# Kernel optimization log

Measured on AMD Instinct MI355X. Metric: run time of the kernel, lower is better.

Reference implementation:

```python
import jax, jax.numpy as jnp
import numpy as np

# Fixed 5-node star graph (edges 0->1,0->2,0->3,0->4) with self-loops,
# GCN symmetric normalization: M[t,s] = deg^-1/2[t] * deg^-1/2[s] over A+I.
# In-degrees: node0 = 1 (self-loop only), nodes 1..4 = 2 (self + edge from 0).
def _prop_matrix():
    M = np.zeros((5, 5), dtype=np.float32)
    M[0, 0] = 1.0
    inv_sqrt2 = 1.0 / np.sqrt(2.0)
    for k in range(1, 5):
        M[k, k] = 0.5            # self-loop: (1/sqrt2)*(1/sqrt2)
        M[k, 0] = inv_sqrt2      # edge 0->k: (1/sqrt1)*(1/sqrt2)
    return jnp.asarray(M)

_M = _prop_matrix()


def _gcn(x, W1, b1, W2, b2):
    # x: [..., 5, 21] node features for batched 5-node graphs
    h = jnp.einsum('ts,...sd->...td', _M, x @ W1) + b1   # [..., 5, 128]
    h = jax.nn.relu(h)
    o = jnp.einsum('ts,...sd->...td', _M, h @ W2) + b2   # [..., 5, 21]
    return o


def setup_inputs() -> dict:
    key = jax.random.key(0)
    k1, k2, k3, k4, k5 = jax.random.split(key, 5)
    B, H, W = 4, 256, 256
    instance_nodes = jax.random.randint(k1, (B, H, W, 5), 0, 129, dtype=jnp.int64)
    class_nodes = jax.random.randint(k2, (21, 5), 0, 129, dtype=jnp.int64)
    emb = jax.random.normal(k3, (129, 21), dtype=jnp.float32)
    emb = emb.at[128].set(0.0)  # padding_idx=128 row is zero
    W1 = jax.random.normal(k4, (21, 128), dtype=jnp.float32) * 0.1
    b1 = jnp.zeros((128,), dtype=jnp.float32)
    W2 = jax.random.normal(k5, (128, 21), dtype=jnp.float32) * 0.1
    b2 = jnp.zeros((21,), dtype=jnp.float32)
    return {"instance_nodes": instance_nodes, "class_nodes": class_nodes,
            "emb": emb, "W1": W1, "b1": b1, "W2": W2, "b2": b2}


def reference(instance_nodes, class_nodes, emb, W1, b1, W2, b2):
    B, H, W, n = instance_nodes.shape
    # class branch: 21 tiny graphs -> [21, 105]
    x_class = emb[class_nodes]                     # [21, 5, 21]
    out_class = _gcn(x_class, W1, b1, W2, b2).reshape(21, 105)
    # instance branch: B*H*W tiny graphs, fully batched
    x_inst = emb[instance_nodes]                   # [B, H, W, 5, 21]
    out_inst = _gcn(x_inst, W1, b1, W2, b2).reshape(B, H, W, 105)
    # inner-product similarity against each class vector
    sim = jnp.einsum('bhwf,cf->bhwc', out_inst, out_class)  # [B, H, W, 21]
    return sim
```

## Files before the change

### kernel.cpp

```cpp
#include <hip/hip_runtime.h>


#define IS2 0.70710678118654752440f

constexpr int NE  = 129;
constexpr int D1  = 128;
constexpr int DF  = 21;
constexpr int NC  = 21;
constexpr int ROWA = 24;

constexpr int U_OFF   = 0;
constexpr int GT_OFF  = U_OFF  + NE * D1;
constexpr int A_OFF   = GT_OFF + D1 * 84;
constexpr int OC_OFF  = A_OFF  + NE * ROWA;
constexpr int S_OFF   = OC_OFF + NC * 105;
constexpr int G0_OFF  = S_OFF  + NC * DF;
constexpr int CST_OFF = G0_OFF + NC * D1;
constexpr int P_OFF   = ((CST_OFF + NC + 31) / 32) * 32;
constexpr long long P_ELEMS32 = 4LL * NE * NE * 32;

constexpr int BT  = 16;
constexpr int NBT = (NE + BT - 1) / BT;

__global__ __launch_bounds__(D1) void k_u(const float* __restrict__ emb,
                                          const float* __restrict__ W1,
                                          float* __restrict__ u) {
    int i = blockIdx.x;
    int j = threadIdx.x;
    __shared__ float e[DF];
    if (threadIdx.x < DF) e[threadIdx.x] = emb[i * DF + threadIdx.x];
    __syncthreads();
    float acc = 0.f;
#pragma unroll
    for (int k = 0; k < DF; ++k) acc += e[k] * W1[k * D1 + j];
    u[i * D1 + j] = acc;
}

__global__ __launch_bounds__(D1) void k_class_a(const int* __restrict__ cn,
                                                const float* __restrict__ b1,
                                                const float* __restrict__ W2,
                                                const float* __restrict__ b2,
                                                float* __restrict__ ws) {
    const float* u = ws + U_OFF;
    float* oc  = ws + OC_OFF;
    float* S   = ws + S_OFF;
    float* cst = ws + CST_OFF;

    const int c   = blockIdx.x;
    const int tid = threadIdx.x;

    __shared__ float h[5 * D1];
    __shared__ float v[5 * DF];
    __shared__ float ocs[105];
    __shared__ float Ss[DF];

    const int n0 = cn[c * 5];
#pragma unroll
    for (int s = 0; s < 5; ++s) {
        int ns = cn[c * 5 + s];
        float pre = (s == 0) ? (u[n0 * D1 + tid] + b1[tid])
                             : (IS2 * u[n0 * D1 + tid] + 0.5f * u[ns * D1 + tid] + b1[tid]);
        h[s * D1 + tid] = fmaxf(pre, 0.f);
    }
    __syncthreads();

    if (tid < 105) {
        int s = tid / DF, j = tid % DF;
        const float* hs = h + s * D1;
        float a0 = 0.f, a1 = 0.f;
#pragma unroll 8
        for (int k = 0; k < D1; k += 2) {
            a0 += hs[k]     * W2[k * DF + j];
            a1 += hs[k + 1] * W2[(k + 1) * DF + j];
        }
        v[tid] = a0 + a1;
    }
    __syncthreads();

    if (tid < 105) {
        int t = tid / DF, j = tid % DF;
        float v0 = v[j];
        float val = (t == 0) ? (v0 + b2[j])
                             : (IS2 * v0 + 0.5f * v[t * DF + j] + b2[j]);
        ocs[tid] = val;
        oc[c * 105 + tid] = val;
    }
    __syncthreads();

    if (tid < DF) {
        float sv = ocs[21 + tid] + ocs[42 + tid] + ocs[63 + tid] + ocs[84 + tid];
        Ss[tid] = sv;
        S[c * DF + tid] = sv;
    }
    __syncthreads();

    if (tid == 0) {
        float acc = 0.f;
#pragma unroll
        for (int j = 0; j < DF; ++j) acc += b2[j] * (ocs[j] + Ss[j]);
        cst[c] = acc;
    }
}

__global__ __launch_bounds__(256) void k_class_b(const float* __restrict__ W2,
                                                 float* __restrict__ ws) {
    const float* oc = ws + OC_OFF;
    const float* S  = ws + S_OFF;
    float* gGt = ws + GT_OFF;
    float* G0  = ws + G0_OFF;

    int idx = blockIdx.x * 256 + threadIdx.x;
    if (idx < D1 * 84) {
        int k = idx / 84, tc = idx % 84;
        int t = tc / DF + 1, c = tc % DF;
        float acc = 0.f;
#pragma unroll
        for (int j = 0; j < DF; ++j) acc += W2[k * DF + j] * oc[c * 105 + t * DF + j];
        gGt[idx] = 0.5f * acc;
    } else if (idx < D1 * 84 + NC * D1) {
        int r = idx - D1 * 84;
        int c = r / D1, k = r % D1;
        float acc = 0.f;
#pragma unroll
        for (int j = 0; j < DF; ++j)
            acc += W2[k * DF + j] * (oc[c * 105 + j] + IS2 * S[c * DF + j]);
        G0[c * D1 + k] = acc;
    }
}

__global__ __launch_bounds__(D1) void k_class_c(const float* __restrict__ b1,
                                                float* __restrict__ ws) {
    const float* u   = ws + U_OFF;
    const float* G0  = ws + G0_OFF;
    const float* cst = ws + CST_OFF;
    float* gA = ws + A_OFF;

    const int n0  = blockIdx.x;
    const int tid = threadIdx.x;

    __shared__ float h0[D1];
    h0[tid] = fmaxf(u[n0 * D1 + tid] + b1[tid], 0.f);
    __syncthreads();

    if (tid < NC) {
        const float* g = G0 + tid * D1;
        float a0 = 0.f, a1 = 0.f;
#pragma unroll 8
        for (int k = 0; k < D1; k += 2) {
            a0 += h0[k]     * g[k];
            a1 += h0[k + 1] * g[k + 1];
        }
        gA[n0 * ROWA + tid] = cst[tid] + a0 + a1;
    }
}

__global__ __launch_bounds__(256) void k_pair(const float* __restrict__ b1,
                                              float* __restrict__ ws, int rowP) {
    const float* u   = ws + U_OFF;
    const float* gGt = ws + GT_OFF;
    float* P         = ws + P_OFF;

    const int a  = blockIdx.x / NBT;
    const int b0 = (blockIdx.x % NBT) * BT;

    __shared__ float ua[D1];
    __shared__ float hp[BT * D1];
    __shared__ float gt[D1 * 84];
    const int tid = threadIdx.x;

    if (tid < D1) ua[tid] = IS2 * u[a * D1 + tid] + b1[tid];
    {
        const float4* src = (const float4*)gGt;
        float4* dst = (float4*)gt;
        for (int i = tid; i < D1 * 84 / 4; i += 256) dst[i] = src[i];
    }
    __syncthreads();

    for (int e = tid; e < BT * D1; e += 256) {
        int p = e / D1, k = e % D1; int b = b0 + p;
        float val = 0.f;
        if (b < NE) val = fmaxf(ua[k] + 0.5f * u[b * D1 + k], 0.f);
        hp[e] = val;
    }
    __syncthreads();

    if (tid < (BT / 2) * 28) {
        const int p0  = (tid / 28) * 2;
        const int tc0 = (tid % 28) * 3;
        const float* hA = hp + p0 * D1;
        const float* hB = hA + D1;

        float e00 = 0.f, e01 = 0.f, e02 = 0.f, e10 = 0.f, e11 = 0.f, e12 = 0.f;
        float o00 = 0.f, o01 = 0.f, o02 = 0.f, o10 = 0.f, o11 = 0.f, o12 = 0.f;
#pragma unroll 4
        for (int k = 0; k < D1; k += 2) {
            float ha0 = hA[k], hb0 = hB[k];
            float ha1 = hA[k + 1], hb1 = hB[k + 1];
            const float* g0 = gt + k * 84 + tc0;
            const float* g1 = g0 + 84;
            float ge0 = g0[0], ge1 = g0[1], ge2 = g0[2];
            float go0 = g1[0], go1 = g1[1], go2 = g1[2];
            e00 += ha0 * ge0; e01 += ha0 * ge1; e02 += ha0 * ge2;
            e10 += hb0 * ge0; e11 += hb0 * ge1; e12 += hb0 * ge2;
            o00 += ha1 * go0; o01 += ha1 * go1; o02 += ha1 * go2;
            o10 += hb1 * go0; o11 += hb1 * go1; o12 += hb1 * go2;
        }

        const int t  = tc0 / DF;
        const int c0 = tc0 - t * DF;
        const long long rbase = (long long)(t * NE * NE + a * NE);
        const int bA = b0 + p0, bB = bA + 1;
        if (bA < NE) {
            float* dst = P + (rbase + bA) * rowP + c0;
            dst[0] = e00 + o00; dst[1] = e01 + o01; dst[2] = e02 + o02;
        }
        if (bB < NE) {
            float* dst = P + (rbase + bB) * rowP + c0;
            dst[0] = e10 + o10; dst[1] = e11 + o11; dst[2] = e12 + o12;
        }
    }
}

__global__ __launch_bounds__(256) void k_main(const int* __restrict__ inst,
                                              const float* __restrict__ ws,
                                              float* __restrict__ out,
                                              long long n_graphs, int rowP) {
    const float* gA = ws + A_OFF;
    const float* P  = ws + P_OFF;

    __shared__ float so[256 * NC];
    __shared__ int   si[256 * 5];
    const int tid = threadIdx.x;
    const long long gbase = (long long)blockIdx.x * 256;
    const bool full = (gbase + 256 <= n_graphs);

    if (full) {
        const int4* src = (const int4*)(inst + gbase * 5);
        int4* dst = (int4*)si;
        for (int i = tid; i < 320; i += 256) dst[i] = src[i];
    } else {
        long long lim = (n_graphs - gbase) * 5;
        for (int i = tid; i < 256 * 5; i += 256)
            si[i] = (i < lim) ? inst[gbase * 5 + i] : 0;
    }
    __syncthreads();

    const long long g = gbase + tid;
    if (g < n_graphs) {
        const int n0 = si[tid * 5 + 0];
        const int n1 = si[tid * 5 + 1];
        const int n2 = si[tid * 5 + 2];
        const int n3 = si[tid * 5 + 3];
        const int n4 = si[tid * 5 + 4];

        const int nn = NE * NE;
        const float4* pa = (const float4*)(gA + n0 * ROWA);
        const float4* p1 = (const float4*)(P + (long long)((0 * nn + n0 * NE + n1)) * rowP);
        const float4* p2 = (const float4*)(P + (long long)((1 * nn + n0 * NE + n2)) * rowP);
        const float4* p3 = (const float4*)(P + (long long)((2 * nn + n0 * NE + n3)) * rowP);
        const float4* p4 = (const float4*)(P + (long long)((3 * nn + n0 * NE + n4)) * rowP);

        float acc[ROWA];
#pragma unroll
        for (int q = 0; q < ROWA / 4; ++q) {
            float4 a0 = pa[q], a1 = p1[q], a2 = p2[q], a3 = p3[q], a4 = p4[q];
            acc[4 * q + 0] = a0.x + a1.x + a2.x + a3.x + a4.x;
            acc[4 * q + 1] = a0.y + a1.y + a2.y + a3.y + a4.y;
            acc[4 * q + 2] = a0.z + a1.z + a2.z + a3.z + a4.z;
            acc[4 * q + 3] = a0.w + a1.w + a2.w + a3.w + a4.w;
        }

#pragma unroll
        for (int c = 0; c < NC; ++c) so[tid * NC + c] = acc[c];
    }
    __syncthreads();

    const long long lim = (n_graphs - gbase) * NC;
    const long long base = gbase * NC;
    for (int i = tid; i < 256 * NC; i += 256)
        if (i < lim) out[base + i] = so[i];
}

extern "C" void kernel_launch(void* const* d_in, const int* in_sizes, int n_in,
                              void* d_out, int out_size, void* d_ws, size_t ws_size,
                              hipStream_t stream) {
    const int*   inst = (const int*)d_in[0];
    const int*   cn   = (const int*)d_in[1];
    const float* emb  = (const float*)d_in[2];
    const float* W1   = (const float*)d_in[3];
    const float* b1   = (const float*)d_in[4];
    const float* W2   = (const float*)d_in[5];
    const float* b2   = (const float*)d_in[6];
    float* out = (float*)d_out;
    float* ws  = (float*)d_ws;

    const long long n_graphs = (long long)in_sizes[0] / 5;
    const int nblk = (int)((n_graphs + 255) / 256);

    const int rowP =
        (ws_size >= (size_t)(P_OFF + P_ELEMS32) * sizeof(float)) ? 32 : 24;

    k_u      <<<dim3(NE),       dim3(D1),  0, stream>>>(emb, W1, ws + U_OFF);
    k_class_a<<<dim3(NC),       dim3(D1),  0, stream>>>(cn, b1, W2, b2, ws);
    k_class_b<<<dim3(53),       dim3(256), 0, stream>>>(W2, ws);
    k_class_c<<<dim3(NE),       dim3(D1),  0, stream>>>(b1, ws);
    k_pair   <<<dim3(NE * NBT), dim3(256), 0, stream>>>(b1, ws, rowP);
    k_main   <<<dim3(nblk),     dim3(256), 0, stream>>>(inst, ws, out, n_graphs, rowP);
}
```

Measured before the change: 144.0 us.

## Split each graph's gather-sum across six threads in main kernel

Changes k_main from one thread per graph (256 graphs per block, staged through shared memory) to six threads per graph (32 graphs per block). Five lanes each gather a float4 from the five precomputed table rows and write their slice of the output directly, and the sixth lane handles the last element. This spreads the random gathers across more threads for more memory-level parallelism and removes the shared-memory output staging. In exchange it issues many more, smaller blocks, makes output stores uncoalesced scalar writes, and leaves some lanes of each wavefront idle.

```diff
diff --git a/kernel.cpp b/kernel.cpp
--- a/kernel.cpp
+++ b/kernel.cpp
@@ -21,6 +21,9 @@
 
 constexpr int BT  = 16;
 constexpr int NBT = (NE + BT - 1) / BT;
+
+constexpr int GPB = 32;
+constexpr int TPG = 6;
 
 __global__ __launch_bounds__(D1) void k_u(const float* __restrict__ emb,
                                           const float* __restrict__ W1,
@@ -221,64 +224,56 @@
     }
 }
 
-__global__ __launch_bounds__(256) void k_main(const int* __restrict__ inst,
-                                              const float* __restrict__ ws,
-                                              float* __restrict__ out,
-                                              long long n_graphs, int rowP) {
+__global__ __launch_bounds__(GPB * TPG) void k_main(const int* __restrict__ inst,
+                                                    const float* __restrict__ ws,
+                                                    float* __restrict__ out,
+                                                    long long n_graphs, int rowP) {
     const float* gA = ws + A_OFF;
     const float* P  = ws + P_OFF;
 
-    __shared__ float so[256 * NC];
-    __shared__ int   si[256 * 5];
+    __shared__ int si[GPB * 5];
     const int tid = threadIdx.x;
-    const long long gbase = (long long)blockIdx.x * 256;
-    const bool full = (gbase + 256 <= n_graphs);
-
-    if (full) {
-        const int4* src = (const int4*)(inst + gbase * 5);
-        int4* dst = (int4*)si;
-        for (int i = tid; i < 320; i += 256) dst[i] = src[i];
+    const long long gbase = (long long)blockIdx.x * GPB;
+
+    if (tid < GPB * 5) {
+        long long lim = (n_graphs - gbase) * 5;
+        si[tid] = (tid < lim) ? inst[gbase * 5 + tid] : 0;
+    }
+    __syncthreads();
+
+    const int gl = tid / TPG;
+    const int q  = tid % TPG;
+    const long long g = gbase + gl;
+    if (g >= n_graphs) return;
+
+    const int n0 = si[gl * 5 + 0];
+    const int n1 = si[gl * 5 + 1];
+    const int n2 = si[gl * 5 + 2];
+    const int n3 = si[gl * 5 + 3];
+    const int n4 = si[gl * 5 + 4];
+
+    const int nn = NE * NE;
+    const float* r0 = gA + n0 * ROWA;
+    const float* r1 = P + (long long)(0 * nn + n0 * NE + n1) * rowP;
+    const float* r2 = P + (long long)(1 * nn + n0 * NE + n2) * rowP;
+    const float* r3 = P + (long long)(2 * nn + n0 * NE + n3) * rowP;
+    const float* r4 = P + (long long)(3 * nn + n0 * NE + n4) * rowP;
+
+    float* og = out + g * NC;
+    if (q < 5) {
+        const int o = q * 4;
+        float4 a0 = *(const float4*)(r0 + o);
+        float4 a1 = *(const float4*)(r1 + o);
+        float4 a2 = *(const float4*)(r2 + o);
+        float4 a3 = *(const float4*)(r3 + o);
+        float4 a4 = *(const float4*)(r4 + o);
+        og[o + 0] = a0.x + a1.x + a2.x + a3.x + a4.x;
+        og[o + 1] = a0.y + a1.y + a2.y + a3.y + a4.y;
+        og[o + 2] = a0.z + a1.z + a2.z + a3.z + a4.z;
+        og[o + 3] = a0.w + a1.w + a2.w + a3.w + a4.w;
     } else {
-        long long lim = (n_graphs - gbase) * 5;
-        for (int i = tid; i < 256 * 5; i += 256)
-            si[i] = (i < lim) ? inst[gbase * 5 + i] : 0;
-    }
-    __syncthreads();
-
-    const long long g = gbase + tid;
-    if (g < n_graphs) {
-        const int n0 = si[tid * 5 + 0];
-        const int n1 = si[tid * 5 + 1];
-        const int n2 = si[tid * 5 + 2];
-        const int n3 = si[tid * 5 + 3];
-        const int n4 = si[tid * 5 + 4];
-
-        const int nn = NE * NE;
-        const float4* pa = (const float4*)(gA + n0 * ROWA);
-        const float4* p1 = (const float4*)(P + (long long)((0 * nn + n0 * NE + n1)) * rowP);
-        const float4* p2 = (const float4*)(P + (long long)((1 * nn + n0 * NE + n2)) * rowP);
-        const float4* p3 = (const float4*)(P + (long long)((2 * nn + n0 * NE + n3)) * rowP);
-        const float4* p4 = (const float4*)(P + (long long)((3 * nn + n0 * NE + n4)) * rowP);
-
-        float acc[ROWA];
-#pragma unroll
-        for (int q = 0; q < ROWA / 4; ++q) {
-            float4 a0 = pa[q], a1 = p1[q], a2 = p2[q], a3 = p3[q], a4 = p4[q];
-            acc[4 * q + 0] = a0.x + a1.x + a2.x + a3.x + a4.x;
-            acc[4 * q + 1] = a0.y + a1.y + a2.y + a3.y + a4.y;
-            acc[4 * q + 2] = a0.z + a1.z + a2.z + a3.z + a4.z;
-            acc[4 * q + 3] = a0.w + a1.w + a2.w + a3.w + a4.w;
-        }
-
-#pragma unroll
-        for (int c = 0; c < NC; ++c) so[tid * NC + c] = acc[c];
-    }
-    __syncthreads();
-
-    const long long lim = (n_graphs - gbase) * NC;
-    const long long base = gbase * NC;
-    for (int i = tid; i < 256 * NC; i += 256)
-        if (i < lim) out[base + i] = so[i];
+        og[20] = r0[20] + r1[20] + r2[20] + r3[20] + r4[20];
+    }
 }
 
 extern "C" void kernel_launch(void* const* d_in, const int* in_sizes, int n_in,
@@ -295,15 +290,15 @@
     float* ws  = (float*)d_ws;
 
     const long long n_graphs = (long long)in_sizes[0] / 5;
-    const int nblk = (int)((n_graphs + 255) / 256);
+    const int nblk_main = (int)((n_graphs + GPB - 1) / GPB);
 
     const int rowP =
         (ws_size >= (size_t)(P_OFF + P_ELEMS32) * sizeof(float)) ? 32 : 24;
 
-    k_u      <<<dim3(NE),       dim3(D1),  0, stream>>>(emb, W1, ws + U_OFF);
-    k_class_a<<<dim3(NC),       dim3(D1),  0, stream>>>(cn, b1, W2, b2, ws);
-    k_class_b<<<dim3(53),       dim3(256), 0, stream>>>(W2, ws);
-    k_class_c<<<dim3(NE),       dim3(D1),  0, stream>>>(b1, ws);
-    k_pair   <<<dim3(NE * NBT), dim3(256), 0, stream>>>(b1, ws, rowP);
-    k_main   <<<dim3(nblk),     dim3(256), 0, stream>>>(inst, ws, out, n_graphs, rowP);
-}
+    k_u      <<<dim3(NE),        dim3(D1),        0, stream>>>(emb, W1, ws + U_OFF);
+    k_class_a<<<dim3(NC),        dim3(D1),        0, stream>>>(cn, b1, W2, b2, ws);
+    k_class_b<<<dim3(53),        dim3(256),       0, stream>>>(W2, ws);
+    k_class_c<<<dim3(NE),        dim3(D1),        0, stream>>>(b1, ws);
+    k_pair   <<<dim3(NE * NBT),  dim3(256),       0, stream>>>(b1, ws, rowP);
+    k_main   <<<dim3(nblk_main), dim3(GPB * TPG), 0, stream>>>(inst, ws, out, n_graphs, rowP);
+}
```

Measured after the change: 127.4 us. -11.5%, faster.
